# Performance work log

Hardware: AMD Instinct MI355X
Metric: run time of the kernel (lower is better)

The kernel has to match this reference:

```python
import jax, jax.numpy as jnp
import numpy as np

# TT-linear: in_features=1024 -> out_features=4096
IN_DIMS = (8, 8, 4, 4)      # m1..m4, prod = 1024
OUT_DIMS = (8, 8, 8, 8)     # n1..n4, prod = 4096
RANKS = (1, 16, 16, 16, 1)  # r0..r4
IN_FEATURES = 1024
OUT_FEATURES = 4096
BATCH, SEQ = 4, 1024


def _init_core(key, shape):
    # uniform(-1,1)/sqrt(fan_in-ish), matching the original's uniform-style init scale
    fan = shape[0] * shape[1]
    return (2.0 * jax.random.uniform(key, shape, dtype=jnp.float32) - 1.0) / np.sqrt(fan).astype(np.float32)


def setup_inputs() -> dict:
    key = jax.random.key(0)
    ks = jax.random.split(key, 6)
    x = jax.random.normal(ks[0], (BATCH, SEQ, IN_FEATURES), dtype=jnp.float32)
    core0 = _init_core(ks[1], (1, 8, 8, 16))    # [r0, m1, n1, r1]
    core1 = _init_core(ks[2], (16, 8, 8, 16))   # [r1, m2, n2, r2]
    core2 = _init_core(ks[3], (16, 4, 8, 16))   # [r2, m3, n3, r3]
    core3 = _init_core(ks[4], (16, 4, 8, 1))    # [r3, m4, n4, r4]
    bias = (2.0 * jax.random.uniform(ks[5], (OUT_FEATURES,), dtype=jnp.float32) - 1.0) / np.sqrt(OUT_FEATURES).astype(np.float32)
    return {"x": x, "core0": core0, "core1": core1, "core2": core2, "core3": core3, "bias": bias}


def reference(x, core0, core1, core2, core3, bias):
    lead = x.shape[:-1]
    # split the feature axis into TT input factors: [T, m1, m2, m3, m4]
    t = x.reshape((-1,) + IN_DIMS)
    c0 = core0[0]        # [m1, n1, r1]   (boundary rank r0 = 1 squeezed)
    c3 = core3[..., 0]   # [r3, m4, n4]   (boundary rank r4 = 1 squeezed)
    # sequential TT core chain: absorb one m_k, emit one n_k per step
    t = jnp.einsum('tijkl,ixp->tjklxp', t, c0)      # [T, m2,m3,m4, n1, r1]
    t = jnp.einsum('tjklxp,pjyq->tklxyq', t, core1)  # [T, m3,m4, n1,n2, r2]
    t = jnp.einsum('tklxyq,qkzr->tlxyzr', t, core2)  # [T, m4, n1,n2,n3, r3]
    t = jnp.einsum('tlxyzr,rlw->txyzw', t, c3)       # [T, n1,n2,n3,n4]
    y = t.reshape(lead + (OUT_FEATURES,)) + bias
    return y
```

## Files before the change

### kernel.cpp

```cpp
#include <hip/hip_runtime.h>
#include <hip/hip_bf16.h>
#include <cstdint>


typedef __bf16 bf16x8 __attribute__((ext_vector_type(8)));
typedef float f32x4 __attribute__((ext_vector_type(4)));

__device__ __forceinline__ void g2lds16(const void* g, void* l) {
    __builtin_amdgcn_global_load_lds(
        (const __attribute__((address_space(1))) void*)g,
        (__attribute__((address_space(3))) void*)l,
        16, 0, 0);
}

__global__ __launch_bounds__(256) void prep(
    const float* __restrict__ x, __bf16* __restrict__ xb,
    const float* __restrict__ c0, const float* __restrict__ c1,
    const float* __restrict__ c2, const float* __restrict__ c3,
    __bf16* __restrict__ wt) {
    const int b = blockIdx.x;
    const int t = threadIdx.x;
    if (b < 2048) {
        const int i = (b * 256 + t) * 8;
        float4 a0 = *(const float4*)(x + i);
        float4 a1 = *(const float4*)(x + i + 4);
        bf16x8 o;
        o[0] = (__bf16)a0.x; o[1] = (__bf16)a0.y; o[2] = (__bf16)a0.z; o[3] = (__bf16)a0.w;
        o[4] = (__bf16)a1.x; o[5] = (__bf16)a1.y; o[6] = (__bf16)a1.z; o[7] = (__bf16)a1.w;
        *(bf16x8*)(xb + i) = o;
        return;
    }
    __shared__ float t12[4][16];
    __shared__ float t123[4][512];
    __shared__ float c3s[512];
    #pragma unroll
    for (int i = t; i < 512; i += 256) c3s[i] = c3[i];
    const int s = t >> 6;
    const int lane = t & 63;
    const int g = (b - 2048) * 4 + s;
    const int m1 = g >> 9, n1 = (g >> 6) & 7, m2 = (g >> 3) & 7, n2 = g & 7;
    __syncthreads();
    if (lane < 16) {
        const int r2 = lane;
        float sum = 0.f;
        #pragma unroll
        for (int r1 = 0; r1 < 16; ++r1)
            sum += c0[(m1 * 8 + n1) * 16 + r1] * c1[((r1 * 8 + m2) * 8 + n2) * 16 + r2];
        t12[s][r2] = sum;
    }
    __syncthreads();
    #pragma unroll
    for (int idx = lane; idx < 512; idx += 64) {
        const int m3 = idx >> 7, n3 = (idx >> 4) & 7, r3 = idx & 15;
        float sum = 0.f;
        #pragma unroll
        for (int r2 = 0; r2 < 16; ++r2)
            sum += t12[s][r2] * c2[((r2 * 4 + m3) * 8 + n3) * 16 + r3];
        t123[s][(m3 * 8 + n3) * 16 + r3] = sum;
    }
    __syncthreads();
    const int n3 = lane >> 3, n4 = lane & 7;
    const int n = ((n1 * 8 + n2) * 8 + n3) * 8 + n4;
    const int kbase = (m1 * 8 + m2) * 16;
    float v[16];
    #pragma unroll
    for (int e = 0; e < 16; ++e) v[e] = 0.f;
    #pragma unroll
    for (int m3 = 0; m3 < 4; ++m3) {
        #pragma unroll
        for (int r3 = 0; r3 < 16; ++r3) {
            const float tv = t123[s][(m3 * 8 + n3) * 16 + r3];
            #pragma unroll
            for (int m4 = 0; m4 < 4; ++m4)
                v[m3 * 4 + m4] += tv * c3s[(r3 * 4 + m4) * 8 + n4];
        }
    }
    bf16x8 lo, hi;
    #pragma unroll
    for (int e = 0; e < 8; ++e) { lo[e] = (__bf16)v[e]; hi[e] = (__bf16)v[8 + e]; }
    *(bf16x8*)(wt + (size_t)n * 1024 + kbase)     = lo;
    *(bf16x8*)(wt + (size_t)n * 1024 + kbase + 8) = hi;
}


#define SCHED() __builtin_amdgcn_sched_barrier(0)
#define BAR()  do { SCHED(); __builtin_amdgcn_s_barrier(); SCHED(); } while (0)
#define WAITVM(n) do { SCHED(); asm volatile("s_waitcnt vmcnt(" #n ")"); SCHED(); } while (0)

__global__ __launch_bounds__(512, 4) void tt_gemm(
    const __bf16* __restrict__ A, const __bf16* __restrict__ B,
    const float* __restrict__ bias, float* __restrict__ C) {
    constexpr int K = 1024, N = 4096;
    constexpr int NKT = 32;
    __shared__ __bf16 sA[3][256 * 32];
    __shared__ __bf16 sB[3][128 * 32];
    const int t = threadIdx.x;
    const int lane = t & 63;
    const int wave = t >> 6;
    const int wm = (wave >> 1) * 64;
    const int wn = (wave & 1) * 64;
    const int l15 = lane & 15, lh = lane >> 4;
    const int cOff = ((lh ^ ((l15 >> 1) & 3)) << 4);

    const int xcd = blockIdx.x & 7;
    const int lid = blockIdx.x >> 3;
    const int bm = ((xcd >> 2) * 8 + (lid & 7)) * 256;
    const int bn = ((xcd & 3) * 8 + (lid >> 3)) * 128;

    const int c0i = t, c1i = t + 512;
    const int rA0 = c0i >> 2, rA1 = c1i >> 2;
    const int lcA0 = (c0i & 3) ^ ((rA0 >> 1) & 3);
    const int lcA1 = (c1i & 3) ^ ((rA1 >> 1) & 3);
    const int rB = t >> 2;
    const int lcB = (t & 3) ^ ((rB >> 1) & 3);
    const __bf16* a0p = A + (size_t)(bm + rA0) * K + lcA0 * 8;
    const __bf16* a1p = A + (size_t)(bm + rA1) * K + lcA1 * 8;
    const __bf16* bp  = B + (size_t)(bn + rB)  * K + lcB * 8;

#define ST(kt, sl) do { \
    g2lds16(a0p + (size_t)(kt) * 32, (char*)&sA[sl][0] + c0i * 16); \
    g2lds16(a1p + (size_t)(kt) * 32, (char*)&sA[sl][0] + c1i * 16); \
    g2lds16(bp  + (size_t)(kt) * 32, (char*)&sB[sl][0] + t * 16); } while (0)
#define LDA(dst, mi) dst = *(const bf16x8*)((const char*)&sA[s0][0] + (wm + (mi) * 16 + l15) * 64 + cOff)
#define LDB(dst, ni) dst = *(const bf16x8*)((const char*)&sB[s0][0] + (wn + (ni) * 16 + l15) * 64 + cOff)

    f32x4 acc[4][4] = {};

    ST(0, 0);
    ST(1, 1);
    WAITVM(3);
    BAR();

    #pragma unroll 1
    for (int kt = 0; kt < NKT; ++kt) {
        const int s0 = kt % 3;
        const int s2 = (kt + 2) % 3;
        bf16x8 af[4], bf[4];
        #pragma unroll
        for (int mi = 0; mi < 4; ++mi) LDA(af[mi], mi);
        #pragma unroll
        for (int ni = 0; ni < 4; ++ni) LDB(bf[ni], ni);
        if (kt < NKT - 2) ST(kt + 2, s2);
        __builtin_amdgcn_s_setprio(1);
        #pragma unroll
        for (int mi = 0; mi < 4; ++mi)
            #pragma unroll
            for (int ni = 0; ni < 4; ++ni)
                acc[mi][ni] = __builtin_amdgcn_mfma_f32_16x16x32_bf16(
                    af[mi], bf[ni], acc[mi][ni], 0, 0, 0);
        __builtin_amdgcn_s_setprio(0);
        if (kt < NKT - 2)       { WAITVM(3); }
        else if (kt == NKT - 2) { WAITVM(0); }
        BAR();
    }

    float bv[4];
    #pragma unroll
    for (int ni = 0; ni < 4; ++ni) bv[ni] = bias[bn + wn + ni * 16 + l15];
    #pragma unroll
    for (int mi = 0; mi < 4; ++mi) {
        #pragma unroll
        for (int r = 0; r < 4; ++r) {
            const int row = bm + wm + mi * 16 + lh * 4 + r;
            float* crow = C + (size_t)row * N + bn + wn + l15;
            #pragma unroll
            for (int ni = 0; ni < 4; ++ni)
                crow[ni * 16] = acc[mi][ni][r] + bv[ni];
        }
    }
#undef ST
#undef LDA
#undef LDB
}

extern "C" void kernel_launch(void* const* d_in, const int* in_sizes, int n_in,
                              void* d_out, int out_size, void* d_ws, size_t ws_size,
                              hipStream_t stream) {
    const float* x    = (const float*)d_in[0];
    const float* c0   = (const float*)d_in[1];
    const float* c1   = (const float*)d_in[2];
    const float* c2   = (const float*)d_in[3];
    const float* c3   = (const float*)d_in[4];
    const float* bias = (const float*)d_in[5];
    float* out = (float*)d_out;

    __bf16* xb = (__bf16*)d_ws;
    __bf16* wt = xb + (size_t)4096 * 1024;

    prep<<<3072, 256, 0, stream>>>(x, xb, c0, c1, c2, c3, wt);
    tt_gemm<<<512, 512, 0, stream>>>(xb, wt, bias, out);
}
```

Measured before the change: 136.5 us.

## Halve GEMM block to 4 waves, each computing a 128x64 tile

The GEMM block shrinks from 8 waves to 4 waves while keeping the 256x128 block tile, so each wave now computes 128x64 outputs with 32 MFMA accumulators instead of 16. Each thread issues twice as many global-to-LDS loads per stage, and the wait counts are adjusted to match. The goal is more MFMA work per LDS fragment load and fewer waves per barrier. The cost is higher register pressure (128 accumulator VGPRs plus 12 fragments), fewer waves to hide latency, and a longer issue stream per thread.

```diff
diff --git a/kernel.cpp b/kernel.cpp
--- a/kernel.cpp
+++ b/kernel.cpp
@@ -87,7 +87,7 @@
 #define BAR()  do { SCHED(); __builtin_amdgcn_s_barrier(); SCHED(); } while (0)
 #define WAITVM(n) do { SCHED(); asm volatile("s_waitcnt vmcnt(" #n ")"); SCHED(); } while (0)
 
-__global__ __launch_bounds__(512, 4) void tt_gemm(
+__global__ __launch_bounds__(256, 2) void tt_gemm(
     const __bf16* __restrict__ A, const __bf16* __restrict__ B,
     const float* __restrict__ bias, float* __restrict__ C) {
     constexpr int K = 1024, N = 4096;
@@ -97,7 +97,7 @@
     const int t = threadIdx.x;
     const int lane = t & 63;
     const int wave = t >> 6;
-    const int wm = (wave >> 1) * 64;
+    const int wm = (wave >> 1) * 128;
     const int wn = (wave & 1) * 64;
     const int l15 = lane & 15, lh = lane >> 4;
     const int cOff = ((lh ^ ((l15 >> 1) & 3)) << 4);
@@ -107,49 +107,60 @@
     const int bm = ((xcd >> 2) * 8 + (lid & 7)) * 256;
     const int bn = ((xcd & 3) * 8 + (lid >> 3)) * 128;
 
-    const int c0i = t, c1i = t + 512;
-    const int rA0 = c0i >> 2, rA1 = c1i >> 2;
-    const int lcA0 = (c0i & 3) ^ ((rA0 >> 1) & 3);
-    const int lcA1 = (c1i & 3) ^ ((rA1 >> 1) & 3);
-    const int rB = t >> 2;
-    const int lcB = (t & 3) ^ ((rB >> 1) & 3);
-    const __bf16* a0p = A + (size_t)(bm + rA0) * K + lcA0 * 8;
-    const __bf16* a1p = A + (size_t)(bm + rA1) * K + lcA1 * 8;
-    const __bf16* bp  = B + (size_t)(bn + rB)  * K + lcB * 8;
+    const __bf16* ap[4];
+    const __bf16* bp[2];
+    #pragma unroll
+    for (int j = 0; j < 4; ++j) {
+        const int c = t + j * 256;
+        const int r = c >> 2;
+        const int lc = (c & 3) ^ ((r >> 1) & 3);
+        ap[j] = A + (size_t)(bm + r) * K + lc * 8;
+    }
+    #pragma unroll
+    for (int j = 0; j < 2; ++j) {
+        const int c = t + j * 256;
+        const int r = c >> 2;
+        const int lc = (c & 3) ^ ((r >> 1) & 3);
+        bp[j] = B + (size_t)(bn + r) * K + lc * 8;
+    }
 
 #define ST(kt, sl) do { \
-    g2lds16(a0p + (size_t)(kt) * 32, (char*)&sA[sl][0] + c0i * 16); \
-    g2lds16(a1p + (size_t)(kt) * 32, (char*)&sA[sl][0] + c1i * 16); \
-    g2lds16(bp  + (size_t)(kt) * 32, (char*)&sB[sl][0] + t * 16); } while (0)
+    _Pragma("unroll") \
+    for (int j = 0; j < 4; ++j) \
+        g2lds16(ap[j] + (size_t)(kt) * 32, (char*)&sA[sl][0] + (t + j * 256) * 16); \
+    _Pragma("unroll") \
+    for (int j = 0; j < 2; ++j) \
+        g2lds16(bp[j] + (size_t)(kt) * 32, (char*)&sB[sl][0] + (t + j * 256) * 16); \
+} while (0)
 #define LDA(dst, mi) dst = *(const bf16x8*)((const char*)&sA[s0][0] + (wm + (mi) * 16 + l15) * 64 + cOff)
 #define LDB(dst, ni) dst = *(const bf16x8*)((const char*)&sB[s0][0] + (wn + (ni) * 16 + l15) * 64 + cOff)
 
-    f32x4 acc[4][4] = {};
+    f32x4 acc[8][4] = {};
 
     ST(0, 0);
     ST(1, 1);
-    WAITVM(3);
+    WAITVM(6);
     BAR();
 
     #pragma unroll 1
     for (int kt = 0; kt < NKT; ++kt) {
         const int s0 = kt % 3;
         const int s2 = (kt + 2) % 3;
-        bf16x8 af[4], bf[4];
-        #pragma unroll
-        for (int mi = 0; mi < 4; ++mi) LDA(af[mi], mi);
+        bf16x8 af[8], bf[4];
+        #pragma unroll
+        for (int mi = 0; mi < 8; ++mi) LDA(af[mi], mi);
         #pragma unroll
         for (int ni = 0; ni < 4; ++ni) LDB(bf[ni], ni);
         if (kt < NKT - 2) ST(kt + 2, s2);
         __builtin_amdgcn_s_setprio(1);
         #pragma unroll
-        for (int mi = 0; mi < 4; ++mi)
+        for (int mi = 0; mi < 8; ++mi)
             #pragma unroll
             for (int ni = 0; ni < 4; ++ni)
                 acc[mi][ni] = __builtin_amdgcn_mfma_f32_16x16x32_bf16(
                     af[mi], bf[ni], acc[mi][ni], 0, 0, 0);
         __builtin_amdgcn_s_setprio(0);
-        if (kt < NKT - 2)       { WAITVM(3); }
+        if (kt < NKT - 2)       { WAITVM(6); }
         else if (kt == NKT - 2) { WAITVM(0); }
         BAR();
     }
@@ -158,7 +169,7 @@
     #pragma unroll
     for (int ni = 0; ni < 4; ++ni) bv[ni] = bias[bn + wn + ni * 16 + l15];
     #pragma unroll
-    for (int mi = 0; mi < 4; ++mi) {
+    for (int mi = 0; mi < 8; ++mi) {
         #pragma unroll
         for (int r = 0; r < 4; ++r) {
             const int row = bm + wm + mi * 16 + lh * 4 + r;
@@ -188,5 +199,5 @@
     __bf16* wt = xb + (size_t)4096 * 1024;
 
     prep<<<3072, 256, 0, stream>>>(x, xb, c0, c1, c2, c3, wt);
-    tt_gemm<<<512, 512, 0, stream>>>(xb, wt, bias, out);
-}
+    tt_gemm<<<512, 256, 0, stream>>>(xb, wt, bias, out);
+}
```

New measurement: 135.8 us. Within noise of the previous version (-0.5%).
